# Kernel tuning notes

Hardware: AMD Instinct MI355X
Metric: run time of the kernel (lower is better)

## Reference

```python
import jax, jax.numpy as jnp
import numpy as np

COMMITMENT_COST = 0.25


def setup_inputs() -> dict:
    key = jax.random.key(0)
    k1, k2 = jax.random.split(key)
    n_embeddings, embedding_dim = 1024, 256
    x = jax.random.normal(k1, (32, 2048, embedding_dim), dtype=jnp.float32)
    r = 1.0 / n_embeddings
    embedding = jax.random.uniform(k2, (n_embeddings, embedding_dim),
                                   dtype=jnp.float32, minval=-r, maxval=r)
    return {"x": x, "embedding": embedding}


def reference(x, embedding):
    M, D = embedding.shape
    # x is detached before flattening in the original quantize()
    x_flat = jax.lax.stop_gradient(x).reshape(-1, D)  # [N, D]
    distances = (jnp.sum(embedding * embedding, axis=1)
                 + jnp.sum(x_flat * x_flat, axis=1, keepdims=True)
                 - 2.0 * (x_flat @ embedding.T))  # [N, M]
    indices = jnp.argmin(distances, axis=-1)  # [N] int
    quantized = embedding[indices].reshape(x.shape)  # gather + view_as(x)
    # commitment loss: quantized is detached in the loss term
    e_latent_loss = jnp.mean(jnp.square(x - jax.lax.stop_gradient(quantized)))
    loss = COMMITMENT_COST * e_latent_loss
    return quantized, loss, indices
```

## Files before the change

kernel.cpp:

```cpp
#include <hip/hip_runtime.h>

#define N_ROWS   65536
#define D        256
#define D4       64
#define M        1024
#define LOSS_OFF 16777216
#define IDX_OFF  16777217
#define COMMIT_SCALE (0.25f / 16777216.0f)
#define E_SCALE  1024.0f
#define C_SCALE  0.001953125f

typedef _Float16 f16x8 __attribute__((ext_vector_type(8)));
typedef _Float16 f16x4 __attribute__((ext_vector_type(4)));
typedef float    f32x4 __attribute__((ext_vector_type(4)));

__device__ __forceinline__ void async_copy16(const void* g, void* l) {
    __builtin_amdgcn_global_load_lds(
        (const __attribute__((address_space(1))) unsigned int*)g,
        (__attribute__((address_space(3))) unsigned int*)l, 16, 0, 0);
}

__device__ __forceinline__ float np_block128(const float* __restrict__ a, int l) {
    float r0 = __fmul_rn(a[l +   0], a[l +   0]);
    float r1 = __fmul_rn(a[l +  16], a[l +  16]);
    float r2 = __fmul_rn(a[l +  32], a[l +  32]);
    float r3 = __fmul_rn(a[l +  48], a[l +  48]);
    float r4 = __fmul_rn(a[l +  64], a[l +  64]);
    float r5 = __fmul_rn(a[l +  80], a[l +  80]);
    float r6 = __fmul_rn(a[l +  96], a[l +  96]);
    float r7 = __fmul_rn(a[l + 112], a[l + 112]);
    return __fadd_rn(__fadd_rn(__fadd_rn(r0, r1), __fadd_rn(r2, r3)),
                     __fadd_rn(__fadd_rn(r4, r5), __fadd_rn(r6, r7)));
}
__device__ __forceinline__ float np_reduce16(float v) {
    float s = __fadd_rn(v, __shfl_down(v, 8));
    s = __fadd_rn(s, __shfl_down(s, 4));
    s = __fadd_rn(s, __shfl_down(s, 2));
    s = __fadd_rn(s, __shfl_down(s, 1));
    return s;
}

__global__ __launch_bounds__(256) void norms_kernel(
    const float4* __restrict__ x4, const float4* __restrict__ emb4,
    float* __restrict__ bsq, float* __restrict__ esq,
    float* __restrict__ loss_slot) {
    __shared__ float rowbuf[16 * 260];
    const int tid = threadIdx.x;
    const float4* src4;
    float* dst;
    int row0;
    if (blockIdx.x < 4096) {
        row0 = blockIdx.x * 16;
        src4 = x4 + (size_t)row0 * 64;
        dst = bsq + row0;
    } else {
        row0 = (blockIdx.x - 4096) * 16;
        src4 = emb4 + (size_t)row0 * 64;
        dst = esq + row0;
    }
    #pragma unroll
    for (int p = 0; p < 4; ++p) {
        const int f = tid + p * 256;
        const int r = f >> 6, c4 = f & 63;
        *(float4*)&rowbuf[r * 260 + c4 * 4] = src4[f];
    }
    __syncthreads();
    const int l = tid & 15, g = tid >> 4;
    const float* base = &rowbuf[g * 260];
    const float v0 = np_block128(base, l);
    const float v1 = np_block128(base + 128, l);
    const float t0 = np_reduce16(v0);
    const float t1 = np_reduce16(v1);
    if (l == 0) dst[g] = __fadd_rn(t0, t1);
    if (blockIdx.x == 0 && tid == 0) *loss_slot = 0.0f;
}

__global__ __launch_bounds__(256) void esplit_kernel(
    const float4* __restrict__ emb4,
    _Float16* __restrict__ e_hi, _Float16* __restrict__ e_mid) {
    const int f = blockIdx.x * 256 + threadIdx.x;
    const int code = f >> 6, k4 = f & 63;
    const int kc = k4 >> 3, ko = (k4 & 7) * 4;
    float4 v = emb4[f];
    float a[4] = {v.x * E_SCALE, v.y * E_SCALE, v.z * E_SCALE, v.w * E_SCALE};
    f16x4 hi, mid;
    #pragma unroll
    for (int j = 0; j < 4; ++j) {
        _Float16 h = (_Float16)a[j];
        float r = __fsub_rn(a[j], (float)h);
        hi[j] = h;
        mid[j] = (_Float16)r;
    }
    const size_t ofs = (size_t)kc * (M * 32) + (size_t)code * 32 + ko;
    *(f16x4*)&e_hi[ofs]  = hi;
    *(f16x4*)&e_mid[ofs] = mid;
}

__global__ __launch_bounds__(256, 2) void argmin_mfma_kernel(
    const float* __restrict__ x,
    const _Float16* __restrict__ e_hi, const _Float16* __restrict__ e_mid,
    const float* __restrict__ esq, const float* __restrict__ bsq,
    float* __restrict__ idx_out_f, int* __restrict__ idx_out_i) {
    __shared__ __attribute__((aligned(16))) _Float16 buf[2][8192];
    __shared__ float red_d[64][2];
    __shared__ int   red_i[64][2];

    const int tid = threadIdx.x;
    const int w = tid >> 6, lane = tid & 63;
    const int w_row = w >> 1, w_col = w & 1;
    const int lm = lane & 15, q = lane >> 4;
    const int row0 = blockIdx.x * 64;

    f16x8 a_hi[2][8], a_mid[2][8];
    #pragma unroll
    for (int fm = 0; fm < 2; ++fm) {
        const float* xr = x + (size_t)(row0 + w_row * 32 + fm * 16 + lm) * D + q * 8;
        #pragma unroll
        for (int kc = 0; kc < 8; ++kc) {
            float4 v0 = *(const float4*)(xr + kc * 32);
            float4 v1 = *(const float4*)(xr + kc * 32 + 4);
            float e[8] = {v0.x, v0.y, v0.z, v0.w, v1.x, v1.y, v1.z, v1.w};
            #pragma unroll
            for (int j = 0; j < 8; ++j) {
                _Float16 h = (_Float16)e[j];
                float r = __fsub_rn(e[j], (float)h);
                a_hi[fm][kc][j]  = h;
                a_mid[fm][kc][j] = (_Float16)r;
            }
        }
    }
    float bq[2][4];
    #pragma unroll
    for (int fm = 0; fm < 2; ++fm)
        #pragma unroll
        for (int r = 0; r < 4; ++r)
            bq[fm][r] = bsq[row0 + w_row * 32 + fm * 16 + q * 4 + r];

    float best[2][4] = {{3.0e38f, 3.0e38f, 3.0e38f, 3.0e38f},
                        {3.0e38f, 3.0e38f, 3.0e38f, 3.0e38f}};
    int bidx[2][4] = {{0, 0, 0, 0}, {0, 0, 0, 0}};

    auto dma = [&](int c, int bsel) {
        const int jt = c >> 3, kc = c & 7;
        const size_t gofs = (size_t)kc * 65536 + (size_t)jt * 8192
                          + (size_t)w * 2048 + (size_t)lane * 16;
        const char* gh = (const char*)e_hi + gofs;
        const char* gm = (const char*)e_mid + gofs;
        _Float16* lh = &buf[bsel][w * 1024];
        _Float16* lmm = &buf[bsel][4096 + w * 1024];
        async_copy16(gh, lh);
        async_copy16(gh + 1024, lh + 512);
        async_copy16(gm, lmm);
        async_copy16(gm + 1024, lmm + 512);
    };

    dma(0, 0);
    for (int jt = 0; jt < 8; ++jt) {
        const int j0 = jt * 128;
        f32x4 acc[2][4] = {};
        for (int kc = 0; kc < 8; ++kc) {
            const int c = jt * 8 + kc;
            __syncthreads();
            if (c < 63) dma(c + 1, (c + 1) & 1);
            const int bsel = c & 1;
            f16x8 bh[4], bm[4];
            #pragma unroll
            for (int fn = 0; fn < 4; ++fn) {
                const int bo = (w_col * 64 + fn * 16 + lm) * 32 + q * 8;
                bh[fn] = *(const f16x8*)&buf[bsel][bo];
                bm[fn] = *(const f16x8*)&buf[bsel][4096 + bo];
            }
            #pragma unroll
            for (int fm = 0; fm < 2; ++fm)
                #pragma unroll
                for (int fn = 0; fn < 4; ++fn) {
                    acc[fm][fn] = __builtin_amdgcn_mfma_f32_16x16x32_f16(
                        a_hi[fm][kc], bh[fn], acc[fm][fn], 0, 0, 0);
                    acc[fm][fn] = __builtin_amdgcn_mfma_f32_16x16x32_f16(
                        a_mid[fm][kc], bh[fn], acc[fm][fn], 0, 0, 0);
                    acc[fm][fn] = __builtin_amdgcn_mfma_f32_16x16x32_f16(
                        a_hi[fm][kc], bm[fn], acc[fm][fn], 0, 0, 0);
                }
        }
        #pragma unroll
        for (int fn = 0; fn < 4; ++fn) {
            const int j = j0 + w_col * 64 + fn * 16 + lm;
            const float eq = esq[j];
            #pragma unroll
            for (int fm = 0; fm < 2; ++fm)
                #pragma unroll
                for (int r = 0; r < 4; ++r) {
                    const float d = __fsub_rn(__fadd_rn(eq, bq[fm][r]),
                                              acc[fm][fn][r] * C_SCALE);
                    if (d < best[fm][r]) { best[fm][r] = d; bidx[fm][r] = j; }
                }
        }
    }
    #pragma unroll
    for (int fm = 0; fm < 2; ++fm)
        #pragma unroll
        for (int r = 0; r < 4; ++r) {
            float d = best[fm][r]; int i = bidx[fm][r];
            #pragma unroll
            for (int mv = 1; mv <= 8; mv <<= 1) {
                const float d2 = __shfl_xor(d, mv, 64);
                const int   i2 = __shfl_xor(i, mv, 64);
                if (d2 < d || (d2 == d && i2 < i)) { d = d2; i = i2; }
            }
            best[fm][r] = d; bidx[fm][r] = i;
        }
    __syncthreads();
    if (lm == 0) {
        #pragma unroll
        for (int fm = 0; fm < 2; ++fm)
            #pragma unroll
            for (int r = 0; r < 4; ++r) {
                const int rl = w_row * 32 + fm * 16 + q * 4 + r;
                red_d[rl][w_col] = best[fm][r];
                red_i[rl][w_col] = bidx[fm][r];
            }
    }
    __syncthreads();
    if (tid < 64) {
        float d0 = red_d[tid][0]; int i0 = red_i[tid][0];
        const float d1 = red_d[tid][1]; const int i1 = red_i[tid][1];
        if (d1 < d0 || (d1 == d0 && i1 < i0)) { d0 = d1; i0 = i1; }
        idx_out_f[row0 + tid] = (float)i0;
        idx_out_i[row0 + tid] = i0;
    }
}

__global__ __launch_bounds__(256) void gather_loss_kernel(
    const float4* __restrict__ x4, const float4* __restrict__ emb4,
    const int* __restrict__ idx, float4* __restrict__ q4,
    float* __restrict__ loss_slot) {
    const int base = blockIdx.x * 256 + threadIdx.x;
    float acc = 0.0f;
    #pragma unroll
    for (int i = 0; i < 16; ++i) {
        const int f   = base + i * (1024 * 256);
        const int row = f >> 6;
        const int c4  = f & 63;
        const int e   = idx[row];
        float4 qv = emb4[e * D4 + c4];
        float4 xv = x4[f];
        q4[f] = qv;
        const float dx = xv.x - qv.x, dy = xv.y - qv.y;
        const float dz = xv.z - qv.z, dw = xv.w - qv.w;
        acc += dx * dx + dy * dy + dz * dz + dw * dw;
    }
    #pragma unroll
    for (int off = 32; off; off >>= 1) acc += __shfl_down(acc, off, 64);
    __shared__ float wsum[4];
    const int lane = threadIdx.x & 63, w = threadIdx.x >> 6;
    if (lane == 0) wsum[w] = acc;
    __syncthreads();
    if (threadIdx.x == 0) {
        atomicAdd(loss_slot, (wsum[0] + wsum[1] + wsum[2] + wsum[3]) * COMMIT_SCALE);
    }
}

extern "C" void kernel_launch(void* const* d_in, const int* in_sizes, int n_in,
                              void* d_out, int out_size, void* d_ws, size_t ws_size,
                              hipStream_t stream) {
    const float* x   = (const float*)d_in[0];
    const float* emb = (const float*)d_in[1];
    float* out = (float*)d_out;
    float*    bsq  = (float*)d_ws;
    float*    esq  = bsq + N_ROWS;
    int*      idx  = (int*)(esq + M);
    _Float16* e_hi = (_Float16*)(idx + N_ROWS);
    _Float16* e_mid = e_hi + (size_t)M * D;

    norms_kernel<<<4096 + M / 16, 256, 0, stream>>>((const float4*)x,
                                                    (const float4*)emb,
                                                    bsq, esq, out + LOSS_OFF);
    esplit_kernel<<<M * D / 4 / 256, 256, 0, stream>>>((const float4*)emb,
                                                       e_hi, e_mid);
    argmin_mfma_kernel<<<N_ROWS / 64, 256, 0, stream>>>(x, e_hi, e_mid,
                                                        esq, bsq,
                                                        out + IDX_OFF, idx);
    gather_loss_kernel<<<1024, 256, 0, stream>>>((const float4*)x,
                                                 (const float4*)emb, idx,
                                                 (float4*)out, out + LOSS_OFF);
}
```

Before: 251.2 us.

## Fuse gather and loss into argmin kernel, swizzle codebook LDS layout

```diff
diff --git a/kernel.cpp b/kernel.cpp
--- a/kernel.cpp
+++ b/kernel.cpp
@@ -48,13 +48,12 @@
     const int tid = threadIdx.x;
     const float4* src4;
     float* dst;
-    int row0;
     if (blockIdx.x < 4096) {
-        row0 = blockIdx.x * 16;
+        const int row0 = blockIdx.x * 16;
         src4 = x4 + (size_t)row0 * 64;
         dst = bsq + row0;
     } else {
-        row0 = (blockIdx.x - 4096) * 16;
+        const int row0 = (blockIdx.x - 4096) * 16;
         src4 = emb4 + (size_t)row0 * 64;
         dst = esq + row0;
     }
@@ -80,7 +79,10 @@
     _Float16* __restrict__ e_hi, _Float16* __restrict__ e_mid) {
     const int f = blockIdx.x * 256 + threadIdx.x;
     const int code = f >> 6, k4 = f & 63;
-    const int kc = k4 >> 3, ko = (k4 & 7) * 4;
+    const int jt = code >> 7, c = code & 127;
+    const int kc = k4 >> 3;
+    const int q  = (k4 & 7) >> 1;
+    const int u  = c * 4 + (q ^ ((c >> 1) & 3));
     float4 v = emb4[f];
     float a[4] = {v.x * E_SCALE, v.y * E_SCALE, v.z * E_SCALE, v.w * E_SCALE};
     f16x4 hi, mid;
@@ -91,19 +93,24 @@
         hi[j] = h;
         mid[j] = (_Float16)r;
     }
-    const size_t ofs = (size_t)kc * (M * 32) + (size_t)code * 32 + ko;
+    const size_t ofs = (size_t)kc * 32768 + (size_t)jt * 4096
+                     + (size_t)u * 8 + (k4 & 1) * 4;
     *(f16x4*)&e_hi[ofs]  = hi;
     *(f16x4*)&e_mid[ofs] = mid;
 }
 
-__global__ __launch_bounds__(256, 2) void argmin_mfma_kernel(
+__global__ __launch_bounds__(256, 1) void argmin_mfma_kernel(
     const float* __restrict__ x,
     const _Float16* __restrict__ e_hi, const _Float16* __restrict__ e_mid,
     const float* __restrict__ esq, const float* __restrict__ bsq,
-    float* __restrict__ idx_out_f, int* __restrict__ idx_out_i) {
+    const float4* __restrict__ emb4,
+    float* __restrict__ idx_out_f, float4* __restrict__ q4,
+    float* __restrict__ loss_slot) {
     __shared__ __attribute__((aligned(16))) _Float16 buf[2][8192];
     __shared__ float red_d[64][2];
     __shared__ int   red_i[64][2];
+    __shared__ int   fin[64];
+    __shared__ float wsum[4];
 
     const int tid = threadIdx.x;
     const int w = tid >> 6, lane = tid & 63;
@@ -146,13 +153,20 @@
                           + (size_t)w * 2048 + (size_t)lane * 16;
         const char* gh = (const char*)e_hi + gofs;
         const char* gm = (const char*)e_mid + gofs;
-        _Float16* lh = &buf[bsel][w * 1024];
+        _Float16* lh  = &buf[bsel][w * 1024];
         _Float16* lmm = &buf[bsel][4096 + w * 1024];
         async_copy16(gh, lh);
         async_copy16(gh + 1024, lh + 512);
         async_copy16(gm, lmm);
         async_copy16(gm + 1024, lmm + 512);
     };
+
+    int bo[4];
+    #pragma unroll
+    for (int fn = 0; fn < 4; ++fn) {
+        const int c = w_col * 64 + fn * 16 + lm;
+        bo[fn] = (c * 4 + (q ^ ((c >> 1) & 3))) * 8;
+    }
 
     dma(0, 0);
     for (int jt = 0; jt < 8; ++jt) {
@@ -166,9 +180,8 @@
             f16x8 bh[4], bm[4];
             #pragma unroll
             for (int fn = 0; fn < 4; ++fn) {
-                const int bo = (w_col * 64 + fn * 16 + lm) * 32 + q * 8;
-                bh[fn] = *(const f16x8*)&buf[bsel][bo];
-                bm[fn] = *(const f16x8*)&buf[bsel][4096 + bo];
+                bh[fn] = *(const f16x8*)&buf[bsel][bo[fn]];
+                bm[fn] = *(const f16x8*)&buf[bsel][4096 + bo[fn]];
             }
             #pragma unroll
             for (int fm = 0; fm < 2; ++fm)
@@ -225,39 +238,32 @@
         float d0 = red_d[tid][0]; int i0 = red_i[tid][0];
         const float d1 = red_d[tid][1]; const int i1 = red_i[tid][1];
         if (d1 < d0 || (d1 == d0 && i1 < i0)) { d0 = d1; i0 = i1; }
+        fin[tid] = i0;
         idx_out_f[row0 + tid] = (float)i0;
-        idx_out_i[row0 + tid] = i0;
-    }
-}
-
-__global__ __launch_bounds__(256) void gather_loss_kernel(
-    const float4* __restrict__ x4, const float4* __restrict__ emb4,
-    const int* __restrict__ idx, float4* __restrict__ q4,
-    float* __restrict__ loss_slot) {
-    const int base = blockIdx.x * 256 + threadIdx.x;
-    float acc = 0.0f;
-    #pragma unroll
-    for (int i = 0; i < 16; ++i) {
-        const int f   = base + i * (1024 * 256);
-        const int row = f >> 6;
-        const int c4  = f & 63;
-        const int e   = idx[row];
-        float4 qv = emb4[e * D4 + c4];
-        float4 xv = x4[f];
-        q4[f] = qv;
+    }
+    __syncthreads();
+
+    const float4* x4 = (const float4*)x;
+    const size_t base4 = (size_t)row0 * D4;
+    float lacc = 0.0f;
+    #pragma unroll
+    for (int p = 0; p < 16; ++p) {
+        const int f = tid + p * 256;
+        const int r = f >> 6, c4 = f & 63;
+        const int e = fin[r];
+        float4 qv = emb4[(size_t)e * D4 + c4];
+        float4 xv = x4[base4 + f];
+        q4[base4 + f] = qv;
         const float dx = xv.x - qv.x, dy = xv.y - qv.y;
         const float dz = xv.z - qv.z, dw = xv.w - qv.w;
-        acc += dx * dx + dy * dy + dz * dz + dw * dw;
-    }
-    #pragma unroll
-    for (int off = 32; off; off >>= 1) acc += __shfl_down(acc, off, 64);
-    __shared__ float wsum[4];
-    const int lane = threadIdx.x & 63, w = threadIdx.x >> 6;
-    if (lane == 0) wsum[w] = acc;
-    __syncthreads();
-    if (threadIdx.x == 0) {
+        lacc += dx * dx + dy * dy + dz * dz + dw * dw;
+    }
+    #pragma unroll
+    for (int off = 32; off; off >>= 1) lacc += __shfl_down(lacc, off, 64);
+    if (lane == 0) wsum[w] = lacc;
+    __syncthreads();
+    if (tid == 0)
         atomicAdd(loss_slot, (wsum[0] + wsum[1] + wsum[2] + wsum[3]) * COMMIT_SCALE);
-    }
 }
 
 extern "C" void kernel_launch(void* const* d_in, const int* in_sizes, int n_in,
@@ -268,8 +274,7 @@
     float* out = (float*)d_out;
     float*    bsq  = (float*)d_ws;
     float*    esq  = bsq + N_ROWS;
-    int*      idx  = (int*)(esq + M);
-    _Float16* e_hi = (_Float16*)(idx + N_ROWS);
+    _Float16* e_hi = (_Float16*)(esq + M);
     _Float16* e_mid = e_hi + (size_t)M * D;
 
     norms_kernel<<<4096 + M / 16, 256, 0, stream>>>((const float4*)x,
@@ -279,8 +284,8 @@
                                                        e_hi, e_mid);
     argmin_mfma_kernel<<<N_ROWS / 64, 256, 0, stream>>>(x, e_hi, e_mid,
                                                         esq, bsq,
-                                                        out + IDX_OFF, idx);
-    gather_loss_kernel<<<1024, 256, 0, stream>>>((const float4*)x,
-                                                 (const float4*)emb, idx,
-                                                 (float4*)out, out + LOSS_OFF);
-}
+                                                        (const float4*)emb,
+                                                        out + IDX_OFF,
+                                                        (float4*)out,
+                                                        out + LOSS_OFF);
+}
```

Measured after the change: 333.7 us. 32.8% more time.
